# Kernel tuning notes

Hardware: AMD Instinct MI355X
Metric: run time of the kernel (lower is better)

Reference implementation:

```python
import jax, jax.numpy as jnp
import numpy as np

NUM_HEADS = 16
N_WIRES = 8  # d_k == n_wires, hard-coded in QLayer


def quantum_heads(x, theta):
    """Exact closed form of the 8-wire circuit: RX-encode + trainable RX + CNOT ring + PauliZ.
    RX(x)RX(t)=RX(x+t); product state -> independent bits with E[(-1)^b_i]=cos(ang_i);
    CNOT ring permutes basis so final-bit XOR subsets give:
      <Z_0> = prod_{i=1..7} cos(ang_i);  <Z_w> = prod_{i=0..w} cos(ang_i) for w>=1.
    """
    B, S, E = x.shape
    ang = x.reshape(B, S, NUM_HEADS, N_WIRES) + theta          # composed RX angles
    c = jnp.cos(ang)                                            # [B,S,H,8]
    cp = jnp.cumprod(c, axis=-1)                                # prefix products
    z0 = jnp.prod(c[..., 1:], axis=-1, keepdims=True)           # wire 0
    z = jnp.concatenate([z0, cp[..., 1:]], axis=-1)             # [B,S,H,8]
    return z.reshape(B, S, E)


def reference(x, theta, W, b):
    B, S, E = x.shape
    d_k = N_WIRES
    proj = quantum_heads(x, theta)                              # q = k = v (same fn of x)
    h = proj.reshape(B, S, NUM_HEADS, d_k).transpose(0, 2, 1, 3)  # [B,H,S,d]
    scores = jnp.einsum('bhqd,bhkd->bhqk', h, h) / jnp.sqrt(jnp.float32(d_k))
    attn = jax.nn.softmax(scores, axis=-1)
    out = jnp.einsum('bhqk,bhkd->bhqd', attn, h)
    out = out.transpose(0, 2, 1, 3).reshape(B, S, E)
    return out @ W.T + b


def setup_inputs() -> dict:
    key = jax.random.key(0)
    k1, k2, k3 = jax.random.split(key, 3)
    B, S, E = 8, 1024, 128
    x = jax.random.normal(k1, (B, S, E), dtype=jnp.float32)
    theta = jax.random.normal(k2, (N_WIRES,), dtype=jnp.float32)
    W = jax.random.normal(k3, (E, E), dtype=jnp.float32) / np.float32(np.sqrt(E))
    b = jnp.zeros((E,), dtype=jnp.float32)
    return {"x": x, "theta": theta, "W": W, "b": b}
```

## Files before the change

kernel.cpp:

```cpp
#include <hip/hip_runtime.h>

#define NHEADS 16
#define NW 8
#define SEQ 1024
#define BATCH 8
#define EMB 128

typedef _Float16 half2_t __attribute__((ext_vector_type(2)));
typedef _Float16 half4_t __attribute__((ext_vector_type(4)));
typedef _Float16 half8_t __attribute__((ext_vector_type(8)));
typedef float    f32x4   __attribute__((ext_vector_type(4)));

__device__ __forceinline__ half2_t pkrtz(float a, float b) {
    return __builtin_bit_cast(half2_t, __builtin_amdgcn_cvt_pkrtz(a, b));
}

#define KVT       8192
#define KVT_STR   1040
#define ONES_OFF  16512
#define ZERO_OFF  16520
#define SMEM_H    16544

__device__ __forceinline__ void qrow(const float* __restrict__ xp,
                                     const float* __restrict__ th, float* z) {
    float4 a = *reinterpret_cast<const float4*>(xp);
    float4 b = *reinterpret_cast<const float4*>(xp + 4);
    float c0 = __cosf(a.x + th[0]);
    float c1 = __cosf(a.y + th[1]);
    float c2 = __cosf(a.z + th[2]);
    float c3 = __cosf(a.w + th[3]);
    float c4 = __cosf(b.x + th[4]);
    float c5 = __cosf(b.y + th[5]);
    float c6 = __cosf(b.z + th[6]);
    float c7 = __cosf(b.w + th[7]);
    float u = c1 * c2;
    u *= c3; u *= c4; u *= c5; u *= c6; u *= c7;
    z[0] = u;
    z[1] = c0 * c1;
    z[2] = z[1] * c2;
    z[3] = z[2] * c3;
    z[4] = z[3] * c4;
    z[5] = z[4] * c5;
    z[6] = z[5] * c6;
    z[7] = z[6] * c7;
}

__global__ __launch_bounds__(256, 4) void qattn_mfma(
    const float* __restrict__ x,
    const float* __restrict__ theta,
    __fp16* __restrict__ P)
{
    __shared__ __align__(16) _Float16 smem[SMEM_H];
    const int t   = threadIdx.x;
    const int bid = blockIdx.x;
    const int qs  = bid & 7;
    const int bh  = bid >> 3;
    const int b   = bh >> 4, h = bh & 15;

    float th[8];
#pragma unroll
    for (int w = 0; w < 8; ++w) th[w] = theta[w];

#pragma unroll
    for (int i = 0; i < 4; ++i) {
        const int kl = t + 256 * i;
        float z[8];
        qrow(x + ((size_t)(b * SEQ + kl) * EMB + h * NW), th, z);
        half8_t hv;
#pragma unroll
        for (int d = 0; d < 8; ++d) hv[d] = (_Float16)z[d];
        *reinterpret_cast<half8_t*>(&smem[kl * 8]) = hv;
#pragma unroll
        for (int d = 0; d < 8; ++d) smem[KVT + d * KVT_STR + kl] = hv[d];
    }
    if (t < 8)              smem[ONES_OFF + t]     = (_Float16)1.0f;
    else if (t < 16)        smem[ZERO_OFF + t - 8] = (_Float16)0.0f;
    __syncthreads();

    const int lane = t & 63;
    const int wv   = t >> 6;
    const int q16  = lane & 15;
    const int qd   = lane >> 4;
    const int qbase = qs * 128 + wv * 32;

    const _Float16 QSh = (_Float16)0.51012924f;
    half8_t qfrag[2];
#pragma unroll
    for (int qi = 0; qi < 2; ++qi) {
        const _Float16* qp = (qd == 0)
            ? &smem[(qbase + qi * 16 + q16) * 8] : &smem[ZERO_OFF];
        half8_t qv = *reinterpret_cast<const half8_t*>(qp);
#pragma unroll
        for (int j = 0; j < 8; ++j) qv[j] = qv[j] * QSh;
        qfrag[qi] = qv;
    }

    const _Float16* ka = (qd == 0) ? &smem[q16 * 8]        : &smem[ZERO_OFF];
    const _Float16* kb = (qd == 0) ? &smem[(16 + q16) * 8] : &smem[ZERO_OFF];
    const int kstep = (qd == 0) ? 256 : 0;
    const _Float16* vp; int vstep;
    if (q16 < 8)       { vp = &smem[KVT + q16 * KVT_STR + qd * 8]; vstep = 32; }
    else if (q16 == 8) { vp = &smem[ONES_OFF]; vstep = 0; }
    else               { vp = &smem[ZERO_OFF]; vstep = 0; }

    const bool oddq = (qd & 1);
    const bool hiC  = (qd >= 2);
    const int  iA   = (q16 + (qd & 1) * 32 + (qd >> 1) * 16) * 4;
    const int  iB   = iA ^ 64;
    const int  lidx = (32 + q16) * 4;

    f32x4 oacc[2] = {{0.f, 0.f, 0.f, 0.f}, {0.f, 0.f, 0.f, 0.f}};
    const f32x4 zc = {0.f, 0.f, 0.f, 0.f};

    half8_t kA = *reinterpret_cast<const half8_t*>(ka);
    half8_t kB = *reinterpret_cast<const half8_t*>(kb);
    half8_t vA = *reinterpret_cast<const half8_t*>(vp);

    for (int kt = 0; kt < 32; ++kt) {
        ka += kstep; kb += kstep; vp += vstep;
        half8_t nkA = *reinterpret_cast<const half8_t*>(ka);
        half8_t nkB = *reinterpret_cast<const half8_t*>(kb);
        half8_t nvA = *reinterpret_cast<const half8_t*>(vp);

#pragma unroll
        for (int qi = 0; qi < 2; ++qi) {
            f32x4 c0 = __builtin_amdgcn_mfma_f32_16x16x32_f16(kA, qfrag[qi], zc, 0, 0, 0);
            f32x4 c1 = __builtin_amdgcn_mfma_f32_16x16x32_f16(kB, qfrag[qi], zc, 0, 0, 0);
            half2_t p0 = pkrtz(__builtin_amdgcn_exp2f(c0[0]), __builtin_amdgcn_exp2f(c0[1]));
            half2_t p1 = pkrtz(__builtin_amdgcn_exp2f(c0[2]), __builtin_amdgcn_exp2f(c0[3]));
            half2_t p2 = pkrtz(__builtin_amdgcn_exp2f(c1[0]), __builtin_amdgcn_exp2f(c1[1]));
            half2_t p3 = pkrtz(__builtin_amdgcn_exp2f(c1[2]), __builtin_amdgcn_exp2f(c1[3]));
            union { half2_t h; int i; } u0, u1, u2, u3;
            u0.h = p0; u1.h = p1; u2.h = p2; u3.h = p3;
            const int a0 = oddq ? u2.i : u0.i;
            const int a1 = oddq ? u3.i : u1.i;
            const int a2 = oddq ? u0.i : u2.i;
            const int a3 = oddq ? u1.i : u3.i;
            const int r0 = __builtin_amdgcn_ds_bpermute(iA, a0);
            const int r1 = __builtin_amdgcn_ds_bpermute(iA, a1);
            const int r2 = __builtin_amdgcn_ds_bpermute(iB, a2);
            const int r3 = __builtin_amdgcn_ds_bpermute(iB, a3);
            union { int i[4]; half8_t h; } bf;
            bf.i[0] = hiC ? r2 : r0;
            bf.i[1] = hiC ? r3 : r1;
            bf.i[2] = hiC ? r0 : r2;
            bf.i[3] = hiC ? r1 : r3;
            oacc[qi] = __builtin_amdgcn_mfma_f32_16x16x32_f16(vA, bf.h, oacc[qi], 0, 0, 0);
        }
        kA = nkA; kB = nkB; vA = nvA;
    }

#pragma unroll
    for (int qi = 0; qi < 2; ++qi) {
        f32x4 c = oacc[qi];
        const float lsum = __int_as_float(
            __builtin_amdgcn_ds_bpermute(lidx, __float_as_int(c[0])));
        const float inv = 1.0f / lsum;
        if (qd < 2) {
            half2_t u0 = pkrtz(c[0] * inv, c[1] * inv);
            half2_t u1 = pkrtz(c[2] * inv, c[3] * inv);
            half4_t o4; o4[0] = u0[0]; o4[1] = u0[1]; o4[2] = u1[0]; o4[3] = u1[1];
            const int row = b * SEQ + qbase + qi * 16 + q16;
            *reinterpret_cast<half4_t*>(
                reinterpret_cast<_Float16*>(P) + (size_t)row * EMB + h * NW + qd * 4) = o4;
        }
    }
}

__global__ __launch_bounds__(256) void wcast(
    const float* __restrict__ W, _Float16* __restrict__ Wh)
{
    const int g = (blockIdx.x * 256 + threadIdx.x) * 4;
    float4 v = *reinterpret_cast<const float4*>(W + g);
    half4_t h;
    h[0] = (_Float16)v.x; h[1] = (_Float16)v.y;
    h[2] = (_Float16)v.z; h[3] = (_Float16)v.w;
    *reinterpret_cast<half4_t*>(Wh + g) = h;
}

__global__ __launch_bounds__(256) void proj_mfma(
    const __fp16* __restrict__ Pv,
    const _Float16* __restrict__ Wh,
    const float* __restrict__ bias,
    float* __restrict__ out)
{
    const _Float16* P = reinterpret_cast<const _Float16*>(Pv);
    const int t    = threadIdx.x;
    const int lane = t & 63;
    const int wv   = t >> 6;
    const int n16  = lane & 15;
    const int qd   = lane >> 4;
    const int row0 = blockIdx.x * 16;
    const int col0 = wv * 32;

    half8_t a[4];
#pragma unroll
    for (int kb = 0; kb < 4; ++kb)
        a[kb] = *reinterpret_cast<const half8_t*>(
            P + (size_t)(row0 + n16) * EMB + kb * 32 + qd * 8);

    const f32x4 zc = {0.f, 0.f, 0.f, 0.f};
#pragma unroll
    for (int et = 0; et < 2; ++et) {
        const int e = col0 + et * 16 + n16;
        f32x4 acc = zc;
#pragma unroll
        for (int kb = 0; kb < 4; ++kb) {
            half8_t bfr = *reinterpret_cast<const half8_t*>(
                Wh + (size_t)e * EMB + kb * 32 + qd * 8);
            acc = __builtin_amdgcn_mfma_f32_16x16x32_f16(a[kb], bfr, acc, 0, 0, 0);
        }
        const float bv = bias[e];
#pragma unroll
        for (int r = 0; r < 4; ++r)
            out[(size_t)(row0 + qd * 4 + r) * EMB + e] = acc[r] + bv;
    }
}

extern "C" void kernel_launch(void* const* d_in, const int* in_sizes, int n_in,
                              void* d_out, int out_size, void* d_ws, size_t ws_size,
                              hipStream_t stream)
{
    const float* x     = (const float*)d_in[0];
    const float* theta = (const float*)d_in[1];
    const float* W     = (const float*)d_in[2];
    const float* bias  = (const float*)d_in[3];
    float* out = (float*)d_out;

    __fp16*   Pw = (__fp16*)d_ws;
    _Float16* Wh = (_Float16*)((char*)d_ws + (size_t)BATCH * SEQ * EMB * 2);

    wcast<<<16, 256, 0, stream>>>(W, Wh);
    qattn_mfma<<<128 * 8, 256, 0, stream>>>(x, theta, Pw);
    proj_mfma<<<BATCH * SEQ / 16, 256, 0, stream>>>(Pw, Wh, bias, out);
}
```

Baseline: 92.84 us.

## Split attention over more query blocks and fold W cast into projection

```diff
diff --git a/kernel.cpp b/kernel.cpp
--- a/kernel.cpp
+++ b/kernel.cpp
@@ -45,7 +45,7 @@
     z[7] = z[6] * c7;
 }
 
-__global__ __launch_bounds__(256, 4) void qattn_mfma(
+__global__ __launch_bounds__(256, 8) void qattn_mfma(
     const float* __restrict__ x,
     const float* __restrict__ theta,
     __fp16* __restrict__ P)
@@ -53,8 +53,8 @@
     __shared__ __align__(16) _Float16 smem[SMEM_H];
     const int t   = threadIdx.x;
     const int bid = blockIdx.x;
-    const int qs  = bid & 7;
-    const int bh  = bid >> 3;
+    const int qs  = bid & 15;
+    const int bh  = bid >> 4;
     const int b   = bh >> 4, h = bh & 15;
 
     float th[8];
@@ -81,18 +81,17 @@
     const int wv   = t >> 6;
     const int q16  = lane & 15;
     const int qd   = lane >> 4;
-    const int qbase = qs * 128 + wv * 32;
+    const int qbase = qs * 64 + wv * 16;
 
     const _Float16 QSh = (_Float16)0.51012924f;
-    half8_t qfrag[2];
-#pragma unroll
-    for (int qi = 0; qi < 2; ++qi) {
+    half8_t qfrag;
+    {
         const _Float16* qp = (qd == 0)
-            ? &smem[(qbase + qi * 16 + q16) * 8] : &smem[ZERO_OFF];
+            ? &smem[(qbase + q16) * 8] : &smem[ZERO_OFF];
         half8_t qv = *reinterpret_cast<const half8_t*>(qp);
 #pragma unroll
         for (int j = 0; j < 8; ++j) qv[j] = qv[j] * QSh;
-        qfrag[qi] = qv;
+        qfrag = qv;
     }
 
     const _Float16* ka = (qd == 0) ? &smem[q16 * 8]        : &smem[ZERO_OFF];
@@ -109,50 +108,48 @@
     const int  iB   = iA ^ 64;
     const int  lidx = (32 + q16) * 4;
 
-    f32x4 oacc[2] = {{0.f, 0.f, 0.f, 0.f}, {0.f, 0.f, 0.f, 0.f}};
+    f32x4 oacc = {0.f, 0.f, 0.f, 0.f};
     const f32x4 zc = {0.f, 0.f, 0.f, 0.f};
 
     half8_t kA = *reinterpret_cast<const half8_t*>(ka);
     half8_t kB = *reinterpret_cast<const half8_t*>(kb);
     half8_t vA = *reinterpret_cast<const half8_t*>(vp);
 
+#pragma unroll 2
     for (int kt = 0; kt < 32; ++kt) {
         ka += kstep; kb += kstep; vp += vstep;
         half8_t nkA = *reinterpret_cast<const half8_t*>(ka);
         half8_t nkB = *reinterpret_cast<const half8_t*>(kb);
         half8_t nvA = *reinterpret_cast<const half8_t*>(vp);
 
-#pragma unroll
-        for (int qi = 0; qi < 2; ++qi) {
-            f32x4 c0 = __builtin_amdgcn_mfma_f32_16x16x32_f16(kA, qfrag[qi], zc, 0, 0, 0);
-            f32x4 c1 = __builtin_amdgcn_mfma_f32_16x16x32_f16(kB, qfrag[qi], zc, 0, 0, 0);
-            half2_t p0 = pkrtz(__builtin_amdgcn_exp2f(c0[0]), __builtin_amdgcn_exp2f(c0[1]));
-            half2_t p1 = pkrtz(__builtin_amdgcn_exp2f(c0[2]), __builtin_amdgcn_exp2f(c0[3]));
-            half2_t p2 = pkrtz(__builtin_amdgcn_exp2f(c1[0]), __builtin_amdgcn_exp2f(c1[1]));
-            half2_t p3 = pkrtz(__builtin_amdgcn_exp2f(c1[2]), __builtin_amdgcn_exp2f(c1[3]));
-            union { half2_t h; int i; } u0, u1, u2, u3;
-            u0.h = p0; u1.h = p1; u2.h = p2; u3.h = p3;
-            const int a0 = oddq ? u2.i : u0.i;
-            const int a1 = oddq ? u3.i : u1.i;
-            const int a2 = oddq ? u0.i : u2.i;
-            const int a3 = oddq ? u1.i : u3.i;
-            const int r0 = __builtin_amdgcn_ds_bpermute(iA, a0);
-            const int r1 = __builtin_amdgcn_ds_bpermute(iA, a1);
-            const int r2 = __builtin_amdgcn_ds_bpermute(iB, a2);
-            const int r3 = __builtin_amdgcn_ds_bpermute(iB, a3);
-            union { int i[4]; half8_t h; } bf;
-            bf.i[0] = hiC ? r2 : r0;
-            bf.i[1] = hiC ? r3 : r1;
-            bf.i[2] = hiC ? r0 : r2;
-            bf.i[3] = hiC ? r1 : r3;
-            oacc[qi] = __builtin_amdgcn_mfma_f32_16x16x32_f16(vA, bf.h, oacc[qi], 0, 0, 0);
-        }
+        f32x4 c0 = __builtin_amdgcn_mfma_f32_16x16x32_f16(kA, qfrag, zc, 0, 0, 0);
+        f32x4 c1 = __builtin_amdgcn_mfma_f32_16x16x32_f16(kB, qfrag, zc, 0, 0, 0);
+        half2_t p0 = pkrtz(__builtin_amdgcn_exp2f(c0[0]), __builtin_amdgcn_exp2f(c0[1]));
+        half2_t p1 = pkrtz(__builtin_amdgcn_exp2f(c0[2]), __builtin_amdgcn_exp2f(c0[3]));
+        half2_t p2 = pkrtz(__builtin_amdgcn_exp2f(c1[0]), __builtin_amdgcn_exp2f(c1[1]));
+        half2_t p3 = pkrtz(__builtin_amdgcn_exp2f(c1[2]), __builtin_amdgcn_exp2f(c1[3]));
+        union { half2_t h; int i; } u0, u1, u2, u3;
+        u0.h = p0; u1.h = p1; u2.h = p2; u3.h = p3;
+        const int a0 = oddq ? u2.i : u0.i;
+        const int a1 = oddq ? u3.i : u1.i;
+        const int a2 = oddq ? u0.i : u2.i;
+        const int a3 = oddq ? u1.i : u3.i;
+        const int r0 = __builtin_amdgcn_ds_bpermute(iA, a0);
+        const int r1 = __builtin_amdgcn_ds_bpermute(iA, a1);
+        const int r2 = __builtin_amdgcn_ds_bpermute(iB, a2);
+        const int r3 = __builtin_amdgcn_ds_bpermute(iB, a3);
+        union { int i[4]; half8_t h; } bf;
+        bf.i[0] = hiC ? r2 : r0;
+        bf.i[1] = hiC ? r3 : r1;
+        bf.i[2] = hiC ? r0 : r2;
+        bf.i[3] = hiC ? r1 : r3;
+        oacc = __builtin_amdgcn_mfma_f32_16x16x32_f16(vA, bf.h, oacc, 0, 0, 0);
+
         kA = nkA; kB = nkB; vA = nvA;
     }
 
-#pragma unroll
-    for (int qi = 0; qi < 2; ++qi) {
-        f32x4 c = oacc[qi];
+    {
+        f32x4 c = oacc;
         const float lsum = __int_as_float(
             __builtin_amdgcn_ds_bpermute(lidx, __float_as_int(c[0])));
         const float inv = 1.0f / lsum;
@@ -160,27 +157,16 @@
             half2_t u0 = pkrtz(c[0] * inv, c[1] * inv);
             half2_t u1 = pkrtz(c[2] * inv, c[3] * inv);
             half4_t o4; o4[0] = u0[0]; o4[1] = u0[1]; o4[2] = u1[0]; o4[3] = u1[1];
-            const int row = b * SEQ + qbase + qi * 16 + q16;
+            const int row = b * SEQ + qbase + q16;
             *reinterpret_cast<half4_t*>(
                 reinterpret_cast<_Float16*>(P) + (size_t)row * EMB + h * NW + qd * 4) = o4;
         }
     }
 }
 
-__global__ __launch_bounds__(256) void wcast(
-    const float* __restrict__ W, _Float16* __restrict__ Wh)
-{
-    const int g = (blockIdx.x * 256 + threadIdx.x) * 4;
-    float4 v = *reinterpret_cast<const float4*>(W + g);
-    half4_t h;
-    h[0] = (_Float16)v.x; h[1] = (_Float16)v.y;
-    h[2] = (_Float16)v.z; h[3] = (_Float16)v.w;
-    *reinterpret_cast<half4_t*>(Wh + g) = h;
-}
-
 __global__ __launch_bounds__(256) void proj_mfma(
     const __fp16* __restrict__ Pv,
-    const _Float16* __restrict__ Wh,
+    const float* __restrict__ W,
     const float* __restrict__ bias,
     float* __restrict__ out)
 {
@@ -206,8 +192,16 @@
         f32x4 acc = zc;
 #pragma unroll
         for (int kb = 0; kb < 4; ++kb) {
-            half8_t bfr = *reinterpret_cast<const half8_t*>(
-                Wh + (size_t)e * EMB + kb * 32 + qd * 8);
+            const float* wp = W + (size_t)e * EMB + kb * 32 + qd * 8;
+            float4 w0 = *reinterpret_cast<const float4*>(wp);
+            float4 w1 = *reinterpret_cast<const float4*>(wp + 4);
+            half2_t h0 = pkrtz(w0.x, w0.y);
+            half2_t h1 = pkrtz(w0.z, w0.w);
+            half2_t h2 = pkrtz(w1.x, w1.y);
+            half2_t h3 = pkrtz(w1.z, w1.w);
+            half8_t bfr;
+            bfr[0] = h0[0]; bfr[1] = h0[1]; bfr[2] = h1[0]; bfr[3] = h1[1];
+            bfr[4] = h2[0]; bfr[5] = h2[1]; bfr[6] = h3[0]; bfr[7] = h3[1];
             acc = __builtin_amdgcn_mfma_f32_16x16x32_f16(a[kb], bfr, acc, 0, 0, 0);
         }
         const float bv = bias[e];
@@ -227,10 +221,8 @@
     const float* bias  = (const float*)d_in[3];
     float* out = (float*)d_out;
 
-    __fp16*   Pw = (__fp16*)d_ws;
-    _Float16* Wh = (_Float16*)((char*)d_ws + (size_t)BATCH * SEQ * EMB * 2);
-
-    wcast<<<16, 256, 0, stream>>>(W, Wh);
-    qattn_mfma<<<128 * 8, 256, 0, stream>>>(x, theta, Pw);
-    proj_mfma<<<BATCH * SEQ / 16, 256, 0, stream>>>(Pw, Wh, bias, out);
-}
+    __fp16* Pw = (__fp16*)d_ws;
+
+    qattn_mfma<<<128 * 16, 256, 0, stream>>>(x, theta, Pw);
+    proj_mfma<<<BATCH * SEQ / 16, 256, 0, stream>>>(Pw, W, bias, out);
+}
```

New measurement: 96.85 us. 4.3% more time.

## Use permlane16_swap for P transpose, remap V layout, fold W cast into projection

Applied to the files above, without the earlier changes.

```diff
diff --git a/kernel.cpp b/kernel.cpp
--- a/kernel.cpp
+++ b/kernel.cpp
@@ -10,16 +10,23 @@
 typedef _Float16 half4_t __attribute__((ext_vector_type(4)));
 typedef _Float16 half8_t __attribute__((ext_vector_type(8)));
 typedef float    f32x4   __attribute__((ext_vector_type(4)));
+typedef int      i32x2   __attribute__((ext_vector_type(2)));
 
 __device__ __forceinline__ half2_t pkrtz(float a, float b) {
     return __builtin_bit_cast(half2_t, __builtin_amdgcn_cvt_pkrtz(a, b));
 }
 
+#if __has_builtin(__builtin_amdgcn_permlane16_swap)
+#define HAVE_PLSWAP 1
+#else
+#define HAVE_PLSWAP 0
+#endif
+
 #define KVT       8192
-#define KVT_STR   1040
-#define ONES_OFF  16512
-#define ZERO_OFF  16520
-#define SMEM_H    16544
+#define KVT_STR   1042
+#define ONES_OFF  (KVT + 8 * KVT_STR)
+#define ZERO_OFF  (ONES_OFF + 8)
+#define SMEM_H    (ZERO_OFF + 72)
 
 __device__ __forceinline__ void qrow(const float* __restrict__ xp,
                                      const float* __restrict__ th, float* z) {
@@ -98,15 +105,31 @@
     const _Float16* ka = (qd == 0) ? &smem[q16 * 8]        : &smem[ZERO_OFF];
     const _Float16* kb = (qd == 0) ? &smem[(16 + q16) * 8] : &smem[ZERO_OFF];
     const int kstep = (qd == 0) ? 256 : 0;
-    const _Float16* vp; int vstep;
-    if (q16 < 8)       { vp = &smem[KVT + q16 * KVT_STR + qd * 8]; vstep = 32; }
-    else if (q16 == 8) { vp = &smem[ONES_OFF]; vstep = 0; }
-    else               { vp = &smem[ZERO_OFF]; vstep = 0; }
-
+
+    const unsigned int* vb; int vo0, vo1, vo2, vo3; int vstep;
+    if (q16 < 8) {
+        vb = reinterpret_cast<const unsigned int*>(&smem[KVT + q16 * KVT_STR]);
+#if HAVE_PLSWAP
+        const int bo = (qd & 1) + (qd >> 1) * 4;
+        vo0 = bo; vo1 = bo + 2; vo2 = bo + 8; vo3 = bo + 10;
+#else
+        vo0 = qd * 4; vo1 = vo0 + 1; vo2 = vo0 + 2; vo3 = vo0 + 3;
+#endif
+        vstep = 16;
+    } else if (q16 == 8) {
+        vb = reinterpret_cast<const unsigned int*>(&smem[ONES_OFF]);
+        vo0 = vo1 = vo2 = vo3 = 0; vstep = 0;
+    } else {
+        vb = reinterpret_cast<const unsigned int*>(&smem[ZERO_OFF]);
+        vo0 = vo1 = vo2 = vo3 = 0; vstep = 0;
+    }
+
+#if !HAVE_PLSWAP
     const bool oddq = (qd & 1);
     const bool hiC  = (qd >= 2);
     const int  iA   = (q16 + (qd & 1) * 32 + (qd >> 1) * 16) * 4;
     const int  iB   = iA ^ 64;
+#endif
     const int  lidx = (32 + q16) * 4;
 
     f32x4 oacc[2] = {{0.f, 0.f, 0.f, 0.f}, {0.f, 0.f, 0.f, 0.f}};
@@ -114,13 +137,16 @@
 
     half8_t kA = *reinterpret_cast<const half8_t*>(ka);
     half8_t kB = *reinterpret_cast<const half8_t*>(kb);
-    half8_t vA = *reinterpret_cast<const half8_t*>(vp);
+    unsigned int v0 = vb[vo0], v1 = vb[vo1], v2 = vb[vo2], v3 = vb[vo3];
 
     for (int kt = 0; kt < 32; ++kt) {
-        ka += kstep; kb += kstep; vp += vstep;
+        ka += kstep; kb += kstep; vb += vstep;
         half8_t nkA = *reinterpret_cast<const half8_t*>(ka);
         half8_t nkB = *reinterpret_cast<const half8_t*>(kb);
-        half8_t nvA = *reinterpret_cast<const half8_t*>(vp);
+        unsigned int nv0 = vb[vo0], nv1 = vb[vo1], nv2 = vb[vo2], nv3 = vb[vo3];
+
+        union { unsigned int i[4]; half8_t h; } vf;
+        vf.i[0] = v0; vf.i[1] = v1; vf.i[2] = v2; vf.i[3] = v3;
 
 #pragma unroll
         for (int qi = 0; qi < 2; ++qi) {
@@ -132,6 +158,13 @@
             half2_t p3 = pkrtz(__builtin_amdgcn_exp2f(c1[2]), __builtin_amdgcn_exp2f(c1[3]));
             union { half2_t h; int i; } u0, u1, u2, u3;
             u0.h = p0; u1.h = p1; u2.h = p2; u3.h = p3;
+            union { int i[4]; half8_t h; } bf;
+#if HAVE_PLSWAP
+            i32x2 s01 = __builtin_amdgcn_permlane16_swap(u0.i, u1.i, false, false);
+            i32x2 s23 = __builtin_amdgcn_permlane16_swap(u2.i, u3.i, false, false);
+            bf.i[0] = s01[0]; bf.i[1] = s01[1];
+            bf.i[2] = s23[0]; bf.i[3] = s23[1];
+#else
             const int a0 = oddq ? u2.i : u0.i;
             const int a1 = oddq ? u3.i : u1.i;
             const int a2 = oddq ? u0.i : u2.i;
@@ -140,14 +173,15 @@
             const int r1 = __builtin_amdgcn_ds_bpermute(iA, a1);
             const int r2 = __builtin_amdgcn_ds_bpermute(iB, a2);
             const int r3 = __builtin_amdgcn_ds_bpermute(iB, a3);
-            union { int i[4]; half8_t h; } bf;
             bf.i[0] = hiC ? r2 : r0;
             bf.i[1] = hiC ? r3 : r1;
             bf.i[2] = hiC ? r0 : r2;
             bf.i[3] = hiC ? r1 : r3;
-            oacc[qi] = __builtin_amdgcn_mfma_f32_16x16x32_f16(vA, bf.h, oacc[qi], 0, 0, 0);
+#endif
+            oacc[qi] = __builtin_amdgcn_mfma_f32_16x16x32_f16(vf.h, bf.h, oacc[qi], 0, 0, 0);
         }
-        kA = nkA; kB = nkB; vA = nvA;
+        kA = nkA; kB = nkB;
+        v0 = nv0; v1 = nv1; v2 = nv2; v3 = nv3;
     }
 
 #pragma unroll
@@ -167,20 +201,9 @@
     }
 }
 
-__global__ __launch_bounds__(256) void wcast(
-    const float* __restrict__ W, _Float16* __restrict__ Wh)
-{
-    const int g = (blockIdx.x * 256 + threadIdx.x) * 4;
-    float4 v = *reinterpret_cast<const float4*>(W + g);
-    half4_t h;
-    h[0] = (_Float16)v.x; h[1] = (_Float16)v.y;
-    h[2] = (_Float16)v.z; h[3] = (_Float16)v.w;
-    *reinterpret_cast<half4_t*>(Wh + g) = h;
-}
-
 __global__ __launch_bounds__(256) void proj_mfma(
     const __fp16* __restrict__ Pv,
-    const _Float16* __restrict__ Wh,
+    const float* __restrict__ W,
     const float* __restrict__ bias,
     float* __restrict__ out)
 {
@@ -206,8 +229,16 @@
         f32x4 acc = zc;
 #pragma unroll
         for (int kb = 0; kb < 4; ++kb) {
-            half8_t bfr = *reinterpret_cast<const half8_t*>(
-                Wh + (size_t)e * EMB + kb * 32 + qd * 8);
+            const float* wp = W + (size_t)e * EMB + kb * 32 + qd * 8;
+            float4 w0 = *reinterpret_cast<const float4*>(wp);
+            float4 w1 = *reinterpret_cast<const float4*>(wp + 4);
+            half2_t h0 = pkrtz(w0.x, w0.y);
+            half2_t h1 = pkrtz(w0.z, w0.w);
+            half2_t h2 = pkrtz(w1.x, w1.y);
+            half2_t h3 = pkrtz(w1.z, w1.w);
+            half8_t bfr;
+            bfr[0] = h0[0]; bfr[1] = h0[1]; bfr[2] = h1[0]; bfr[3] = h1[1];
+            bfr[4] = h2[0]; bfr[5] = h2[1]; bfr[6] = h3[0]; bfr[7] = h3[1];
             acc = __builtin_amdgcn_mfma_f32_16x16x32_f16(a[kb], bfr, acc, 0, 0, 0);
         }
         const float bv = bias[e];
@@ -227,10 +258,8 @@
     const float* bias  = (const float*)d_in[3];
     float* out = (float*)d_out;
 
-    __fp16*   Pw = (__fp16*)d_ws;
-    _Float16* Wh = (_Float16*)((char*)d_ws + (size_t)BATCH * SEQ * EMB * 2);
-
-    wcast<<<16, 256, 0, stream>>>(W, Wh);
+    __fp16* Pw = (__fp16*)d_ws;
+
     qattn_mfma<<<128 * 8, 256, 0, stream>>>(x, theta, Pw);
-    proj_mfma<<<BATCH * SEQ / 16, 256, 0, stream>>>(Pw, Wh, bias, out);
-}
+    proj_mfma<<<BATCH * SEQ / 16, 256, 0, stream>>>(Pw, W, bias, out);
+}
```

After: 89.37 us. -3.7%, faster.
